# Performance work log

Hardware: AMD Instinct MI355X
Metric: run time of the kernel (lower is better)

Reference implementation:

```python
import jax, jax.numpy as jnp
import numpy as np

B, H, SQ, SK, D = 2, 16, 2048, 2048, 128
P_DROP = 0.5


def setup_inputs() -> dict:
    key = jax.random.key(0)
    kq, kk, kv, km = jax.random.split(key, 4)
    query = jax.random.normal(kq, (B, H, SQ, D), dtype=jnp.float32)
    key_t = jax.random.normal(kk, (B, H, SK, D), dtype=jnp.float32)
    value = jax.random.normal(kv, (B, H, SK, D), dtype=jnp.float32)
    # deterministic Bernoulli(0.5) keep-mask standing in for dropout(p=0.5, train=True)
    dropout_mask = jax.random.randint(km, (B, H, SQ, SK), 0, 2, dtype=jnp.int32)
    return {"query": query, "key": key_t, "value": value, "dropout_mask": dropout_mask}


def reference(query, key, value, dropout_mask):
    d = query.shape[-1]
    # original: scaled_qk = qk.div(d ** -0.5)  ==  qk * sqrt(d)  (faithful to source)
    scale = jnp.asarray(d, query.dtype) ** 0.5
    qk = jnp.einsum("bhqd,bhkd->bhqk", query, key)  # [B,H,SQ,SK]
    scaled_qk = qk * scale
    keep_scale = jnp.asarray(1.0 / (1.0 - P_DROP), query.dtype)
    dropped = jnp.where(dropout_mask == 1, scaled_qk * keep_scale, jnp.zeros((), query.dtype))
    out = jnp.einsum("bhqk,bhkd->bhqd", dropped, value)  # [B,H,SQ,D]
    return out
```

## Files before the change

kernel.cpp:

```cpp
#include <hip/hip_runtime.h>
#include <hip/hip_bf16.h>

#define B_   2
#define H_   16
#define SQ_  2048
#define SK_  2048
#define D_   128
#define QT   128
#define KT   64
#define NITER (SK_/KT)

using bf16x8 = __attribute__((ext_vector_type(8))) __bf16;
using bf16x4 = __attribute__((ext_vector_type(4))) __bf16;
using f32x4  = __attribute__((ext_vector_type(4))) float;
using i32x4  = __attribute__((ext_vector_type(4))) int;

#define MFMA16(a,b,c) __builtin_amdgcn_mfma_f32_16x16x32_bf16(a,b,c,0,0,0)

#define QOFF 0u
#define KOFF (1u<<25)
#define VOFF (1u<<26)

#define KPITCH 136
#define VPITCH 72
#define PPITCH 72
#define KB_BYTES (KT*KPITCH*2)
#define VB_BYTES (D_*VPITCH*2)
#define PB_BYTES (QT*PPITCH*2)

__device__ __forceinline__ bf16x8 mask8(bf16x8 p, i32x4 a, i32x4 b) {
    bf16x8 r;
    r[0] = a[0] ? p[0] : (__bf16)0.0f;
    r[1] = a[1] ? p[1] : (__bf16)0.0f;
    r[2] = a[2] ? p[2] : (__bf16)0.0f;
    r[3] = a[3] ? p[3] : (__bf16)0.0f;
    r[4] = b[0] ? p[4] : (__bf16)0.0f;
    r[5] = b[1] ? p[5] : (__bf16)0.0f;
    r[6] = b[2] ? p[6] : (__bf16)0.0f;
    r[7] = b[3] ? p[7] : (__bf16)0.0f;
    return r;
}

__global__ __launch_bounds__(256)
void cast_qk(const float* __restrict__ Q, const float* __restrict__ K,
             char* __restrict__ ws)
{
    const size_t idx = (size_t)blockIdx.x * 256 + threadIdx.x;
    const float4* q4 = (const float4*)Q;
    const float4* k4 = (const float4*)K;
    bf16x4* qd = (bf16x4*)(ws + QOFF);
    bf16x4* kd = (bf16x4*)(ws + KOFF);
    #pragma unroll
    for (int i = 0; i < 4; ++i) {
        size_t f = idx + (size_t)i * 524288;
        float4 a = q4[f];
        qd[f] = (bf16x4){ (__bf16)a.x, (__bf16)a.y, (__bf16)a.z, (__bf16)a.w };
        float4 b = k4[f];
        kd[f] = (bf16x4){ (__bf16)b.x, (__bf16)b.y, (__bf16)b.z, (__bf16)b.w };
    }
}

__global__ __launch_bounds__(256)
void transpose_v(const float* __restrict__ V, char* __restrict__ ws)
{
    __shared__ __align__(16) __bf16 vlds[64 * 132];
    const int blk = blockIdx.x;
    const int t   = threadIdx.x;

    const float4* src = (const float4*)(V + (size_t)blk * KT * D_);
    #pragma unroll
    for (int i = 0; i < 8; ++i) {
        int f = t + 256 * i;
        float4 v = src[f];
        int row = f >> 5, col = f & 31;
        *(bf16x4*)&vlds[row * 132 + col * 4] =
            (bf16x4){ (__bf16)v.x, (__bf16)v.y, (__bf16)v.z, (__bf16)v.w };
    }
    __syncthreads();

    __bf16* dst = (__bf16*)(ws + VOFF) + (size_t)blk * (D_ * KT);
    const int d = t >> 1, h = t & 1;
    #pragma unroll
    for (int c = 0; c < 4; ++c) {
        bf16x8 frag;
        #pragma unroll
        for (int j = 0; j < 8; ++j) frag[j] = vlds[(h * 32 + c * 8 + j) * 132 + d];
        *(bf16x8*)&dst[d * KT + h * 32 + c * 8] = frag;
    }
}

__global__ __launch_bounds__(256, 2)
void attn_drop_kernel(const char* __restrict__ ws,
                      const int*  __restrict__ M,
                      float* __restrict__ Out)
{
    __shared__ __align__(16) char smem[KB_BYTES + VB_BYTES + PB_BYTES];
    __bf16* Kb = (__bf16*)smem;
    __bf16* Vb = (__bf16*)(smem + KB_BYTES);
    __bf16* Pb = (__bf16*)(smem + KB_BYTES + VB_BYTES);

    const int tid  = threadIdx.x;
    const int wave = tid >> 6;
    const int lane = tid & 63;
    const int quad = lane >> 4;
    const int ln   = lane & 15;

    const int bh = blockIdx.x >> 4;
    const int qb = blockIdx.x & 15;

    const __bf16* Qbf = (const __bf16*)(ws + QOFF);
    const __bf16* Kbf = (const __bf16*)(ws + KOFF);
    const __bf16* Vtt = (const __bf16*)(ws + VOFF);
    const int* mbase = M + ((size_t)bh * SQ_ + (size_t)qb * QT) * SK_;
    float* optr = Out + ((size_t)bh * SQ_ + (size_t)qb * QT) * D_;

    bf16x8 qf[2][4];
    #pragma unroll
    for (int rt = 0; rt < 2; ++rt)
        #pragma unroll
        for (int s = 0; s < 4; ++s)
            qf[rt][s] = *(const bf16x8*)&Qbf[((size_t)bh*SQ_ + qb*QT + 32*wave + 16*rt + ln)*D_ + 32*s + 8*quad];

    f32x4 Oacc[2][8];
    #pragma unroll
    for (int rt = 0; rt < 2; ++rt)
        #pragma unroll
        for (int dt = 0; dt < 8; ++dt)
            Oacc[rt][dt] = (f32x4){0.f, 0.f, 0.f, 0.f};

    bf16x8 kreg[4], vreg[4];
    {
        const __bf16* kp = Kbf + ((size_t)bh*SK_ + 0*KT) * D_;
        const __bf16* vp = Vtt + (size_t)(bh*32 + 0) * (D_*KT);
        #pragma unroll
        for (int j = 0; j < 4; ++j) {
            kreg[j] = *(const bf16x8*)&kp[j*2048 + tid*8];
            vreg[j] = *(const bf16x8*)&vp[j*2048 + tid*8];
        }
    }

    #pragma unroll 1
    for (int kt = 0; kt < NITER; ++kt) {
        __syncthreads();
        #pragma unroll
        for (int j = 0; j < 4; ++j) {
            *(bf16x8*)&Kb[(16*j + (tid>>4))*KPITCH + (tid&15)*8] = kreg[j];
            *(bf16x8*)&Vb[(32*j + (tid>>3))*VPITCH + (tid&7)*8]  = vreg[j];
        }
        __syncthreads();

        i32x4 mreg[2][2][2];
        #pragma unroll
        for (int rt = 0; rt < 2; ++rt)
            #pragma unroll
            for (int ks = 0; ks < 2; ++ks)
                #pragma unroll
                for (int i = 0; i < 2; ++i)
                    mreg[rt][ks][i] = __builtin_nontemporal_load(
                        (const i32x4*)&mbase[(size_t)(32*wave + 16*rt + ln)*SK_ + kt*KT + 32*ks + 8*quad + 4*i]);

        {
            const int nkt = (kt + 1 < NITER) ? kt + 1 : NITER - 1;
            const __bf16* kp = Kbf + ((size_t)bh*SK_ + nkt*KT) * D_;
            const __bf16* vp = Vtt + (size_t)(bh*32 + nkt) * (D_*KT);
            #pragma unroll
            for (int j = 0; j < 4; ++j) {
                kreg[j] = *(const bf16x8*)&kp[j*2048 + tid*8];
                vreg[j] = *(const bf16x8*)&vp[j*2048 + tid*8];
            }
        }

        f32x4 S[2][4];
        #pragma unroll
        for (int rt = 0; rt < 2; ++rt)
            #pragma unroll
            for (int ct = 0; ct < 4; ++ct)
                S[rt][ct] = (f32x4){0.f, 0.f, 0.f, 0.f};

        #pragma unroll
        for (int s = 0; s < 4; ++s)
            #pragma unroll
            for (int ct = 0; ct < 4; ++ct) {
                bf16x8 kf = *(const bf16x8*)&Kb[(16*ct + ln)*KPITCH + 32*s + 8*quad];
                S[0][ct] = MFMA16(qf[0][s], kf, S[0][ct]);
                S[1][ct] = MFMA16(qf[1][s], kf, S[1][ct]);
            }

        #pragma unroll
        for (int rt = 0; rt < 2; ++rt)
            #pragma unroll
            for (int ct = 0; ct < 4; ++ct) {
                int row0 = 32*wave + 16*rt + 4*quad;
                #pragma unroll
                for (int r = 0; r < 4; ++r)
                    Pb[(row0 + r)*PPITCH + 16*ct + ln] = (__bf16)S[rt][ct][r];
            }

        #pragma unroll
        for (int ks = 0; ks < 2; ++ks) {
            bf16x8 pf0 = mask8(*(const bf16x8*)&Pb[(32*wave +      ln)*PPITCH + 32*ks + 8*quad],
                               mreg[0][ks][0], mreg[0][ks][1]);
            bf16x8 pf1 = mask8(*(const bf16x8*)&Pb[(32*wave + 16 + ln)*PPITCH + 32*ks + 8*quad],
                               mreg[1][ks][0], mreg[1][ks][1]);
            #pragma unroll
            for (int dt = 0; dt < 8; ++dt) {
                bf16x8 vf = *(const bf16x8*)&Vb[(16*dt + ln)*VPITCH + 32*ks + 8*quad];
                Oacc[0][dt] = MFMA16(pf0, vf, Oacc[0][dt]);
                Oacc[1][dt] = MFMA16(pf1, vf, Oacc[1][dt]);
            }
        }
    }

    const float SCALE = 22.62741699796952f;
    #pragma unroll
    for (int rt = 0; rt < 2; ++rt)
        #pragma unroll
        for (int dt = 0; dt < 8; ++dt) {
            int row0 = 32*wave + 16*rt + 4*quad;
            #pragma unroll
            for (int r = 0; r < 4; ++r)
                optr[(size_t)(row0 + r)*D_ + 16*dt + ln] = Oacc[rt][dt][r] * SCALE;
        }
}

extern "C" void kernel_launch(void* const* d_in, const int* in_sizes, int n_in,
                              void* d_out, int out_size, void* d_ws, size_t ws_size,
                              hipStream_t stream) {
    (void)in_sizes; (void)n_in; (void)ws_size; (void)out_size;
    const float* Q = (const float*)d_in[0];
    const float* K = (const float*)d_in[1];
    const float* V = (const float*)d_in[2];
    const int*   M = (const int*)d_in[3];
    float* Out = (float*)d_out;
    char* ws = (char*)d_ws;

    cast_qk<<<dim3(2048), 256, 0, stream>>>(Q, K, ws);
    transpose_v<<<dim3(B_*H_*(SK_/KT)), 256, 0, stream>>>(V, ws);
    attn_drop_kernel<<<dim3(B_*H_*(SQ_/QT)), 256, 0, stream>>>(ws, M, Out);
}
```

Before: 803.2 us.

## Double-buffer dropout mask loads one tile ahead and fuse prep kernels

Result: slower. 824.4 us (+2.6%).

```diff
diff --git a/kernel.cpp b/kernel.cpp
--- a/kernel.cpp
+++ b/kernel.cpp
@@ -42,50 +42,47 @@
 }
 
 __global__ __launch_bounds__(256)
-void cast_qk(const float* __restrict__ Q, const float* __restrict__ K,
-             char* __restrict__ ws)
-{
-    const size_t idx = (size_t)blockIdx.x * 256 + threadIdx.x;
-    const float4* q4 = (const float4*)Q;
-    const float4* k4 = (const float4*)K;
-    bf16x4* qd = (bf16x4*)(ws + QOFF);
-    bf16x4* kd = (bf16x4*)(ws + KOFF);
-    #pragma unroll
-    for (int i = 0; i < 4; ++i) {
-        size_t f = idx + (size_t)i * 524288;
-        float4 a = q4[f];
-        qd[f] = (bf16x4){ (__bf16)a.x, (__bf16)a.y, (__bf16)a.z, (__bf16)a.w };
-        float4 b = k4[f];
-        kd[f] = (bf16x4){ (__bf16)b.x, (__bf16)b.y, (__bf16)b.z, (__bf16)b.w };
-    }
-}
-
-__global__ __launch_bounds__(256)
-void transpose_v(const float* __restrict__ V, char* __restrict__ ws)
+void prep(const float* __restrict__ Q, const float* __restrict__ K,
+          const float* __restrict__ V, char* __restrict__ ws)
 {
     __shared__ __align__(16) __bf16 vlds[64 * 132];
     const int blk = blockIdx.x;
     const int t   = threadIdx.x;
 
-    const float4* src = (const float4*)(V + (size_t)blk * KT * D_);
-    #pragma unroll
-    for (int i = 0; i < 8; ++i) {
-        int f = t + 256 * i;
-        float4 v = src[f];
-        int row = f >> 5, col = f & 31;
-        *(bf16x4*)&vlds[row * 132 + col * 4] =
-            (bf16x4){ (__bf16)v.x, (__bf16)v.y, (__bf16)v.z, (__bf16)v.w };
-    }
-    __syncthreads();
-
-    __bf16* dst = (__bf16*)(ws + VOFF) + (size_t)blk * (D_ * KT);
-    const int d = t >> 1, h = t & 1;
-    #pragma unroll
-    for (int c = 0; c < 4; ++c) {
-        bf16x8 frag;
-        #pragma unroll
-        for (int j = 0; j < 8; ++j) frag[j] = vlds[(h * 32 + c * 8 + j) * 132 + d];
-        *(bf16x8*)&dst[d * KT + h * 32 + c * 8] = frag;
+    {
+        const float4* q4 = (const float4*)Q;
+        const float4* k4 = (const float4*)K;
+        bf16x4* qd = (bf16x4*)(ws + QOFF);
+        bf16x4* kd = (bf16x4*)(ws + KOFF);
+        #pragma unroll
+        for (int i = 0; i < 8; ++i) {
+            size_t f = (size_t)blk * 2048 + t + 256 * i;
+            float4 a = q4[f];
+            qd[f] = (bf16x4){ (__bf16)a.x, (__bf16)a.y, (__bf16)a.z, (__bf16)a.w };
+            float4 b = k4[f];
+            kd[f] = (bf16x4){ (__bf16)b.x, (__bf16)b.y, (__bf16)b.z, (__bf16)b.w };
+        }
+    }
+    {
+        const float4* src = (const float4*)(V + (size_t)blk * KT * D_);
+        #pragma unroll
+        for (int i = 0; i < 8; ++i) {
+            int f = t + 256 * i;
+            float4 v = src[f];
+            int row = f >> 5, col = f & 31;
+            *(bf16x4*)&vlds[row * 132 + col * 4] =
+                (bf16x4){ (__bf16)v.x, (__bf16)v.y, (__bf16)v.z, (__bf16)v.w };
+        }
+        __syncthreads();
+        __bf16* dst = (__bf16*)(ws + VOFF) + (size_t)blk * (D_ * KT);
+        const int d = t >> 1, h = t & 1;
+        #pragma unroll
+        for (int c = 0; c < 4; ++c) {
+            bf16x8 frag;
+            #pragma unroll
+            for (int j = 0; j < 8; ++j) frag[j] = vlds[(h * 32 + c * 8 + j) * 132 + d];
+            *(bf16x8*)&dst[d * KT + h * 32 + c * 8] = frag;
+        }
     }
 }
 
@@ -129,18 +126,28 @@
             Oacc[rt][dt] = (f32x4){0.f, 0.f, 0.f, 0.f};
 
     bf16x8 kreg[4], vreg[4];
+    i32x4  mreg[2][2][2][2];
     {
-        const __bf16* kp = Kbf + ((size_t)bh*SK_ + 0*KT) * D_;
-        const __bf16* vp = Vtt + (size_t)(bh*32 + 0) * (D_*KT);
+        const __bf16* kp = Kbf + (size_t)bh * SK_ * D_;
+        const __bf16* vp = Vtt + (size_t)(bh * 32) * (D_ * KT);
         #pragma unroll
         for (int j = 0; j < 4; ++j) {
             kreg[j] = *(const bf16x8*)&kp[j*2048 + tid*8];
             vreg[j] = *(const bf16x8*)&vp[j*2048 + tid*8];
         }
-    }
-
-    #pragma unroll 1
+        #pragma unroll
+        for (int rt = 0; rt < 2; ++rt)
+            #pragma unroll
+            for (int ks = 0; ks < 2; ++ks)
+                #pragma unroll
+                for (int i = 0; i < 2; ++i)
+                    mreg[0][rt][ks][i] = __builtin_nontemporal_load(
+                        (const i32x4*)&mbase[(size_t)(32*wave + 16*rt + ln)*SK_ + 32*ks + 8*quad + 4*i]);
+    }
+
+    #pragma unroll 2
     for (int kt = 0; kt < NITER; ++kt) {
+        const int par = kt & 1;
         __syncthreads();
         #pragma unroll
         for (int j = 0; j < 4; ++j) {
@@ -149,18 +156,8 @@
         }
         __syncthreads();
 
-        i32x4 mreg[2][2][2];
-        #pragma unroll
-        for (int rt = 0; rt < 2; ++rt)
-            #pragma unroll
-            for (int ks = 0; ks < 2; ++ks)
-                #pragma unroll
-                for (int i = 0; i < 2; ++i)
-                    mreg[rt][ks][i] = __builtin_nontemporal_load(
-                        (const i32x4*)&mbase[(size_t)(32*wave + 16*rt + ln)*SK_ + kt*KT + 32*ks + 8*quad + 4*i]);
-
         {
-            const int nkt = (kt + 1 < NITER) ? kt + 1 : NITER - 1;
+            const int nkt = (kt + 1 < NITER) ? kt + 1 : kt;
             const __bf16* kp = Kbf + ((size_t)bh*SK_ + nkt*KT) * D_;
             const __bf16* vp = Vtt + (size_t)(bh*32 + nkt) * (D_*KT);
             #pragma unroll
@@ -168,6 +165,14 @@
                 kreg[j] = *(const bf16x8*)&kp[j*2048 + tid*8];
                 vreg[j] = *(const bf16x8*)&vp[j*2048 + tid*8];
             }
+            #pragma unroll
+            for (int rt = 0; rt < 2; ++rt)
+                #pragma unroll
+                for (int ks = 0; ks < 2; ++ks)
+                    #pragma unroll
+                    for (int i = 0; i < 2; ++i)
+                        mreg[par^1][rt][ks][i] = __builtin_nontemporal_load(
+                            (const i32x4*)&mbase[(size_t)(32*wave + 16*rt + ln)*SK_ + nkt*KT + 32*ks + 8*quad + 4*i]);
         }
 
         f32x4 S[2][4];
@@ -199,9 +204,9 @@
         #pragma unroll
         for (int ks = 0; ks < 2; ++ks) {
             bf16x8 pf0 = mask8(*(const bf16x8*)&Pb[(32*wave +      ln)*PPITCH + 32*ks + 8*quad],
-                               mreg[0][ks][0], mreg[0][ks][1]);
+                               mreg[par][0][ks][0], mreg[par][0][ks][1]);
             bf16x8 pf1 = mask8(*(const bf16x8*)&Pb[(32*wave + 16 + ln)*PPITCH + 32*ks + 8*quad],
-                               mreg[1][ks][0], mreg[1][ks][1]);
+                               mreg[par][1][ks][0], mreg[par][1][ks][1]);
             #pragma unroll
             for (int dt = 0; dt < 8; ++dt) {
                 bf16x8 vf = *(const bf16x8*)&Vb[(16*dt + ln)*VPITCH + 32*ks + 8*quad];
@@ -219,7 +224,8 @@
             int row0 = 32*wave + 16*rt + 4*quad;
             #pragma unroll
             for (int r = 0; r < 4; ++r)
-                optr[(size_t)(row0 + r)*D_ + 16*dt + ln] = Oacc[rt][dt][r] * SCALE;
+                __builtin_nontemporal_store(Oacc[rt][dt][r] * SCALE,
+                    &optr[(size_t)(row0 + r)*D_ + 16*dt + ln]);
         }
 }
 
@@ -234,7 +240,6 @@
     float* Out = (float*)d_out;
     char* ws = (char*)d_ws;
 
-    cast_qk<<<dim3(2048), 256, 0, stream>>>(Q, K, ws);
-    transpose_v<<<dim3(B_*H_*(SK_/KT)), 256, 0, stream>>>(V, ws);
+    prep<<<dim3(B_*H_*(SK_/KT)), 256, 0, stream>>>(Q, K, V, ws);
     attn_drop_kernel<<<dim3(B_*H_*(SQ_/QT)), 256, 0, stream>>>(ws, M, Out);
 }
```
